# Kernel tuning notes

Measured on AMD Instinct MI355X. Metric: run time of the kernel, lower is better.

Reference implementation:

```python
import jax, jax.numpy as jnp
import numpy as np


def _mab(Q, K, wq, bq, wk, bk, wv, bv, wo, bo, num_heads):
    # Faithful MAB (no LayerNorm: ln=False throughout SetPooler's settrans).
    V = wq.shape[1]
    dh = V // num_heads
    q = Q @ wq + bq          # [..., Sq, V]
    k = K @ wk + bk          # [..., Sk, V]
    v = K @ wv + bv
    def heads(x):
        return x.reshape(*x.shape[:-1], num_heads, dh).swapaxes(-2, -3)  # [..., h, S, dh]
    qh, kh, vh = heads(q), heads(k), heads(v)
    scale = jnp.asarray(1.0 / np.sqrt(V), q.dtype)  # note: torch code scales by sqrt(dim_V), not sqrt(head_dim)
    A = jax.nn.softmax(jnp.einsum('...hqd,...hkd->...hqk', qh, kh) * scale, axis=-1)
    O = qh + jnp.einsum('...hqk,...hkd->...hqd', A, vh)               # residual on Q_
    O = O.swapaxes(-2, -3).reshape(*Q.shape[:-1], V)                  # merge heads back
    return O + jax.nn.relu(O @ wo + bo)


def _forward(rep_R, GA,
             sab0_wq, sab0_bq, sab0_wk, sab0_bk, sab0_wv, sab0_bv, sab0_wo, sab0_bo,
             sab1_wq, sab1_bq, sab1_wk, sab1_bk, sab1_wv, sab1_bv, sab1_wo, sab1_bo,
             pma_S, pma_wq, pma_bq, pma_wk, pma_bk, pma_wv, pma_bv, pma_wo, pma_bo,
             mlp_w1, mlp_b1, mlp_w2, mlp_b2, mlp_w3, mlp_b3):
    # masked mul: GA [G,N] -> [1,G,N,1] broadcast against rep_R [B,G,N,D]
    X = GA[None, :, :, None] * rep_R
    # two SABs (self-attention), 4 heads each
    X = _mab(X, X, sab0_wq, sab0_bq, sab0_wk, sab0_bk, sab0_wv, sab0_bv, sab0_wo, sab0_bo, 4)
    X = _mab(X, X, sab1_wq, sab1_bq, sab1_wk, sab1_bk, sab1_wv, sab1_bv, sab1_wo, sab1_bo, 4)
    # PMA: 1 learned seed, 2 heads, squeeze_out
    S = jnp.broadcast_to(pma_S, (*X.shape[:-2], *pma_S.shape))  # [B,G,1,D]
    O = _mab(S, X, pma_wq, pma_bq, pma_wk, pma_bk, pma_wv, pma_bv, pma_wo, pma_bo, 2)
    O = O[..., 0, :]  # squeeze_out -> [B,G,D]
    # MLP head: D -> 512 -> 512 -> 2*dim_z
    h = jax.nn.relu(O @ mlp_w1 + mlp_b1)
    h = jax.nn.relu(h @ mlp_w2 + mlp_b2)
    return h @ mlp_w3 + mlp_b3


def setup_inputs() -> dict:
    key = jax.random.key(0)
    B, G, N, D = 4, 16, 512, 256
    dz2 = 256  # 2 * dim_z
    ks = iter(jax.random.split(key, 64))
    def lin(fi, fo):
        w = jax.random.normal(next(ks), (fi, fo), jnp.float32) / np.float32(np.sqrt(fi))
        return w, jnp.zeros((fo,), jnp.float32)
    inp = {}
    inp['rep_R'] = jax.random.normal(next(ks), (B, G, N, D), jnp.float32)
    inp['GA'] = jax.random.uniform(next(ks), (G, N), jnp.float32)
    for i in range(2):
        for nm in ('q', 'k', 'v', 'o'):
            w, b = lin(D, D)
            inp[f'sab{i}_w{nm}'] = w
            inp[f'sab{i}_b{nm}'] = b
    inp['pma_S'] = jax.random.normal(next(ks), (1, D), jnp.float32) * np.float32(np.sqrt(6.0 / (1 + D)))
    for nm in ('q', 'k', 'v', 'o'):
        w, b = lin(D, D)
        inp[f'pma_w{nm}'] = w
        inp[f'pma_b{nm}'] = b
    inp['mlp_w1'], inp['mlp_b1'] = lin(D, 512)
    inp['mlp_w2'], inp['mlp_b2'] = lin(512, 512)
    inp['mlp_w3'], inp['mlp_b3'] = lin(512, dz2)
    return inp


def reference(rep_R, GA,
              sab0_wq, sab0_bq, sab0_wk, sab0_bk, sab0_wv, sab0_bv, sab0_wo, sab0_bo,
              sab1_wq, sab1_bq, sab1_wk, sab1_bk, sab1_wv, sab1_bv, sab1_wo, sab1_bo,
              pma_S, pma_wq, pma_bq, pma_wk, pma_bk, pma_wv, pma_bv, pma_wo, pma_bo,
              mlp_w1, mlp_b1, mlp_w2, mlp_b2, mlp_w3, mlp_b3):
    return _forward(rep_R, GA,
                    sab0_wq, sab0_bq, sab0_wk, sab0_bk, sab0_wv, sab0_bv, sab0_wo, sab0_bo,
                    sab1_wq, sab1_bq, sab1_wk, sab1_bk, sab1_wv, sab1_bv, sab1_wo, sab1_bo,
                    pma_S, pma_wq, pma_bq, pma_wk, pma_bk, pma_wv, pma_bv, pma_wo, pma_bo,
                    mlp_w1, mlp_b1, mlp_w2, mlp_b2, mlp_w3, mlp_b3)
```

## Files before the change

kernel.cpp:

```cpp
#include <hip/hip_runtime.h>
#include <hip/hip_bf16.h>

typedef __attribute__((ext_vector_type(4)))  float  f32x4;
typedef __attribute__((ext_vector_type(8)))  __bf16 bf16x8;
typedef __attribute__((ext_vector_type(4)))  __bf16 bf16x4;

#define LOG2E_O16 0.09016844005556021f

__device__ __forceinline__ void gload_lds16(const void* g, void* l) {
  __builtin_amdgcn_global_load_lds(
      (const __attribute__((address_space(1))) void*)g,
      (__attribute__((address_space(3))) void*)l, 16, 0, 0);
}

__global__ __launch_bounds__(256) void scale_kernel(
    const float* __restrict__ rep, const float* __restrict__ GA, __bf16* __restrict__ X)
{
  size_t i = (size_t)blockIdx.x * 256 + threadIdx.x;
  size_t e = i * 4;
  f32x4 r = *(const f32x4*)(rep + e);
  int dn = (int)(e >> 8);
  int n  = dn & 511;
  int g  = (dn >> 9) & 15;
  float ga = GA[g * 512 + n];
  bf16x4 o;
  o[0] = (__bf16)(r[0] * ga); o[1] = (__bf16)(r[1] * ga);
  o[2] = (__bf16)(r[2] * ga); o[3] = (__bf16)(r[3] * ga);
  *(bf16x4*)(X + e) = o;
}

struct WPtrs { const float* w[10]; };
__global__ __launch_bounds__(256) void wconv_kernel(WPtrs ws, __bf16* __restrict__ out)
{
  __shared__ float t[64][65];
  const float* w = ws.w[blockIdx.y];
  __bf16* o = out + (size_t)blockIdx.y * 65536;
  const int tr = (blockIdx.x & 3) * 64, tc = (blockIdx.x >> 2) * 64;
  const int r4 = threadIdx.x >> 6, c = threadIdx.x & 63;
#pragma unroll
  for (int p = 0; p < 16; ++p) {
    int row = p * 4 + r4;
    t[row][c] = w[(size_t)(tr + row) * 256 + tc + c];
  }
  __syncthreads();
#pragma unroll
  for (int p = 0; p < 16; ++p) {
    int row = p * 4 + r4;
    o[(size_t)(tc + row) * 256 + tr + c] = (__bf16)t[c][row];
  }
}

#define STAGE_T(A_, B_, bmv, bnv, Kv, tt, bb) do {                                 \
    _Pragma("unroll")                                                              \
    for (int r = 0; r < 4; ++r) {                                                  \
      int rowl = r * 32 + (tid >> 3);                                              \
      int sl = (tid & 7) ^ (rowl & 7);                                             \
      gload_lds16((const char*)((A_) + (size_t)((bmv) + rowl) * (Kv) + (tt) * 64) + sl * 16, \
                  (char*)sA + (bb) * 16384 + r * 4096 + wv * 1024);                \
      gload_lds16((const char*)((B_) + (size_t)((bnv) + rowl) * (Kv) + (tt) * 64) + sl * 16, \
                  (char*)sB + (bb) * 16384 + r * 4096 + wv * 1024);                \
    } } while (0)

#define GEMM64_PIPE(A_, B_, bmv, bnv, Kv)                                          \
  f32x4 acc[4][4] = {};                                                            \
  const int nt = (Kv) >> 6;                                                        \
  STAGE_T(A_, B_, bmv, bnv, Kv, 0, 0);                                             \
  asm volatile("s_waitcnt vmcnt(0)" ::: "memory");                                 \
  __builtin_amdgcn_s_barrier();                                                    \
  for (int t = 0; t < nt; ++t) {                                                   \
    if (t + 1 < nt) STAGE_T(A_, B_, bmv, bnv, Kv, t + 1, (t + 1) & 1);             \
    const char* bA = (const char*)sA + (t & 1) * 16384;                            \
    const char* bB = (const char*)sB + (t & 1) * 16384;                            \
    bf16x8 af[4][2], bfr[4][2];                                                    \
    _Pragma("unroll")                                                              \
    for (int mi = 0; mi < 4; ++mi) {                                               \
      int row = wr + mi * 16 + l16;                                                \
      _Pragma("unroll")                                                            \
      for (int kk = 0; kk < 2; ++kk) {                                             \
        int sl = (kk * 4 + lg) ^ (row & 7);                                        \
        af[mi][kk] = *(const bf16x8*)(bA + row * 128 + sl * 16);                   \
      }                                                                            \
    }                                                                              \
    _Pragma("unroll")                                                              \
    for (int ni = 0; ni < 4; ++ni) {                                               \
      int row = wc + ni * 16 + l16;                                                \
      _Pragma("unroll")                                                            \
      for (int kk = 0; kk < 2; ++kk) {                                             \
        int sl = (kk * 4 + lg) ^ (row & 7);                                        \
        bfr[ni][kk] = *(const bf16x8*)(bB + row * 128 + sl * 16);                  \
      }                                                                            \
    }                                                                              \
    _Pragma("unroll")                                                              \
    for (int kk = 0; kk < 2; ++kk)                                                 \
      _Pragma("unroll")                                                            \
      for (int mi = 0; mi < 4; ++mi)                                               \
        _Pragma("unroll")                                                          \
        for (int ni = 0; ni < 4; ++ni)                                             \
          acc[mi][ni] = __builtin_amdgcn_mfma_f32_16x16x32_bf16(                   \
              af[mi][kk], bfr[ni][kk], acc[mi][ni], 0, 0, 0);                      \
    asm volatile("s_waitcnt vmcnt(0)" ::: "memory");                               \
    __builtin_amdgcn_s_barrier();                                                  \
  }

struct QKV3 {
  const __bf16* Bt[3];
  const float* bias[3];
  __bf16* out[3];
};

template<int NW>
__global__ __launch_bounds__(256) void gemmqkv_kernel(
    const __bf16* __restrict__ A, QKV3 args, int K)
{
  __shared__ __align__(16) __bf16 smem[32768];
  __bf16* const sA = smem;
  __bf16* const sB = smem + 16384;
  __bf16* const sC = smem;
  const int tid = threadIdx.x, lane = tid & 63, wv = tid >> 6;
  const int l16 = lane & 15, lg = lane >> 4;
  const int wr = (wv >> 1) * 64, wc = (wv & 1) * 64;

  const int nblk = gridDim.x, cpx = nblk >> 3, orig = blockIdx.x;
  const int wg  = (orig & 7) * cpx + (orig >> 3);
  const int r_  = wg / (2 * NW), rem = wg % (2 * NW);
  const int j   = rem >> 1;
  const int bm  = r_ * 128, bn = (rem & 1) * 128;
  const __bf16* __restrict__ Bt = args.Bt[j];

  GEMM64_PIPE(A, Bt, bm, bn, K)

  const float* bias = args.bias[j];
  __bf16* C = args.out[j];
#pragma unroll
  for (int mi = 0; mi < 4; ++mi)
#pragma unroll
    for (int ni = 0; ni < 4; ++ni) {
      int cl = wc + ni * 16 + l16;
      float bval = bias[bn + cl];
      int r0 = wr + mi * 16 + lg * 4;
#pragma unroll
      for (int i = 0; i < 4; ++i)
        sC[(r0 + i) * 136 + cl] = (__bf16)(acc[mi][ni][i] + bval);
    }
  __syncthreads();
#pragma unroll
  for (int it = 0; it < 8; ++it) {
    int idx = it * 256 + tid;
    int r = idx >> 4, seg = idx & 15;
    bf16x8 cv = *(const bf16x8*)&sC[r * 136 + seg * 8];
    *(bf16x8*)(C + (size_t)(bm + r) * 256 + bn + seg * 8) = cv;
  }
}

__global__ __launch_bounds__(256) void gemm128_kernel(
    const __bf16* __restrict__ A, const __bf16* __restrict__ Bt,
    const float* __restrict__ bias, const __bf16* __restrict__ R,
    __bf16* __restrict__ C, int K)
{
  __shared__ __align__(16) __bf16 smem[32768];
  __bf16* const sA = smem;
  __bf16* const sB = smem + 16384;
  __bf16* const sC = smem;
  const int tid = threadIdx.x, lane = tid & 63, wv = tid >> 6;
  const int l16 = lane & 15, lg = lane >> 4;
  const int wr = (wv >> 1) * 64, wc = (wv & 1) * 64;

  const int nblk = gridDim.x, cpx = nblk >> 3, orig = blockIdx.x;
  const int wg  = (orig & 7) * cpx + (orig >> 3);
  const int bm  = (wg >> 1) * 128, bn = (wg & 1) * 128;

  GEMM64_PIPE(A, Bt, bm, bn, K)

  const float* __restrict__ biasp = bias;
#pragma unroll
  for (int mi = 0; mi < 4; ++mi)
#pragma unroll
    for (int ni = 0; ni < 4; ++ni) {
      int cl = wc + ni * 16 + l16;
      float bval = biasp[bn + cl];
      int r0 = wr + mi * 16 + lg * 4;
#pragma unroll
      for (int i = 0; i < 4; ++i)
        sC[(r0 + i) * 136 + cl] = (__bf16)fmaxf(acc[mi][ni][i] + bval, 0.f);
    }
  __syncthreads();
#pragma unroll
  for (int it = 0; it < 8; ++it) {
    int idx = it * 256 + tid;
    int r = idx >> 4, seg = idx & 15;
    bf16x8 cv = *(const bf16x8*)&sC[r * 136 + seg * 8];
    bf16x8 rv = *(const bf16x8*)(R + (size_t)(bm + r) * 256 + bn + seg * 8);
    bf16x8 ov;
#pragma unroll
    for (int i = 0; i < 8; ++i)
      ov[i] = (__bf16)((float)rv[i] + (float)cv[i]);
    *(bf16x8*)(C + (size_t)(bm + r) * 256 + bn + seg * 8) = ov;
  }
}

template<int EPI, bool OUTF32>
__global__ __launch_bounds__(256) void gemm_kernel(
    const __bf16* __restrict__ A, const float* __restrict__ B,
    const float* __restrict__ bias, const __bf16* __restrict__ R,
    void* __restrict__ Cv, int M, int N, int K)
{
  __shared__ __bf16 sA[64][40];
  __shared__ __bf16 sB[64][40];
  const int tid  = threadIdx.x;
  const int lane = tid & 63;
  const int wv   = tid >> 6;
  const int wr   = (wv >> 1) * 32;
  const int wc   = (wv & 1) * 32;
  const int bm   = blockIdx.x * 64;
  const int bn   = blockIdx.y * 64;
  const int l16  = lane & 15;
  const int lk8  = (lane >> 4) * 8;

  const int a_r = tid >> 2, a_c = (tid & 3) * 8;
  const int b_c = tid & 63, b_k = (tid >> 6) * 8;

  f32x4 acc[2][2] = {};

  for (int k0 = 0; k0 < K; k0 += 32) {
    bf16x8 av = *(const bf16x8*)(A + (size_t)(bm + a_r) * K + k0 + a_c);
    float bvf[8];
#pragma unroll
    for (int j = 0; j < 8; ++j)
      bvf[j] = B[(size_t)(k0 + b_k + j) * N + bn + b_c];
    *(bf16x8*)&sA[a_r][a_c] = av;
    bf16x8 bb;
#pragma unroll
    for (int j = 0; j < 8; ++j) bb[j] = (__bf16)bvf[j];
    *(bf16x8*)&sB[b_c][b_k] = bb;
    __syncthreads();
    bf16x8 af0 = *(const bf16x8*)&sA[wr + l16][lk8];
    bf16x8 af1 = *(const bf16x8*)&sA[wr + 16 + l16][lk8];
    bf16x8 bf0 = *(const bf16x8*)&sB[wc + l16][lk8];
    bf16x8 bf1 = *(const bf16x8*)&sB[wc + 16 + l16][lk8];
    acc[0][0] = __builtin_amdgcn_mfma_f32_16x16x32_bf16(af0, bf0, acc[0][0], 0, 0, 0);
    acc[0][1] = __builtin_amdgcn_mfma_f32_16x16x32_bf16(af0, bf1, acc[0][1], 0, 0, 0);
    acc[1][0] = __builtin_amdgcn_mfma_f32_16x16x32_bf16(af1, bf0, acc[1][0], 0, 0, 0);
    acc[1][1] = __builtin_amdgcn_mfma_f32_16x16x32_bf16(af1, bf1, acc[1][1], 0, 0, 0);
    __syncthreads();
  }

#pragma unroll
  for (int mi = 0; mi < 2; ++mi)
#pragma unroll
    for (int ni = 0; ni < 2; ++ni) {
      int col = bn + wc + ni * 16 + l16;
      float bval = bias[col];
      int row0 = bm + wr + mi * 16 + (lane >> 4) * 4;
#pragma unroll
      for (int i = 0; i < 4; ++i) {
        int row = row0 + i;
        float v = acc[mi][ni][i] + bval;
        if (EPI == 1) v = fmaxf(v, 0.f);
        if (EPI == 2) v = (float)R[(size_t)row * N + col] + fmaxf(v, 0.f);
        if (OUTF32) ((float*)Cv)[(size_t)row * N + col] = v;
        else        ((__bf16*)Cv)[(size_t)row * N + col] = (__bf16)v;
      }
    }
}

__global__ __launch_bounds__(512, 2) void attn_sab_kernel(
    __bf16* __restrict__ Q, const __bf16* __restrict__ Kb, const __bf16* __restrict__ Vb)
{
  __shared__ __align__(16) __bf16 sK[128][72];
  __shared__ __align__(16) __bf16 sV[64][136];
  __shared__ __align__(16) __bf16 sP[8][16][72];

  const int orig = blockIdx.x;
  const int wg   = (orig & 7) * 64 + (orig >> 3);
  const int qh   = wg & 1;
  const int pair = wg >> 1;
  const int head = pair & 3;
  const int item = pair >> 2;

  const int tid  = threadIdx.x;
  const int lane = tid & 63;
  const int wv   = tid >> 6;
  const int l16  = lane & 15;
  const int lg   = lane >> 4;
  const size_t base = (size_t)item * (512 * 256) + (size_t)head * 64;
  const int qrow0 = qh * 256 + wv * 32;

  bf16x8 aq[2][2];
#pragma unroll
  for (int qb = 0; qb < 2; ++qb) {
    const size_t qrow = base + (size_t)(qrow0 + qb * 16 + l16) * 256;
    aq[qb][0] = *(const bf16x8*)(Q + qrow + lg * 8);
    aq[qb][1] = *(const bf16x8*)(Q + qrow + 32 + lg * 8);
  }

  f32x4 acco[2][4] = {};
  float lsum[2] = {0.f, 0.f};

  const int kr  = tid >> 3, kc8 = (tid & 7) * 8;
  const int vch = tid & 63, vk8 = (tid >> 6) * 8;

  bf16x8 kreg[2], vreg[2];

#define LOADC(cc) do {                                                             \
    _Pragma("unroll")                                                              \
    for (int p = 0; p < 2; ++p) {                                                  \
      kreg[p] = *(const bf16x8*)(Kb + base + (size_t)((cc)*128 + p*64 + kr)*256 + kc8); \
      bf16x8 vv;                                                                   \
      _Pragma("unroll")                                                            \
      for (int jj = 0; jj < 8; ++jj)                                               \
        vv[jj] = Vb[base + (size_t)((cc)*128 + p*64 + vk8 + jj)*256 + vch];        \
      vreg[p] = vv;                                                                \
    } } while (0)

  LOADC(0);

  for (int c = 0; c < 4; ++c) {
    if (c) __syncthreads();
#pragma unroll
    for (int p = 0; p < 2; ++p) {
      *(bf16x8*)&sK[p * 64 + kr][kc8] = kreg[p];
      *(bf16x8*)&sV[vch][p * 64 + vk8] = vreg[p];
    }
    __syncthreads();
    if (c < 3) LOADC(c + 1);

#pragma unroll
    for (int half = 0; half < 2; ++half) {
      bf16x8 kf0[4], kf1[4];
#pragma unroll
      for (int st = 0; st < 4; ++st) {
        int krl = half * 64 + st * 16 + l16;
        kf0[st] = *(const bf16x8*)&sK[krl][lg * 8];
        kf1[st] = *(const bf16x8*)&sK[krl][32 + lg * 8];
      }
      bf16x8 vf[2][4];
#pragma unroll
      for (int kk = 0; kk < 2; ++kk)
#pragma unroll
        for (int vt = 0; vt < 4; ++vt)
          vf[kk][vt] = *(const bf16x8*)&sV[vt * 16 + l16][half * 64 + kk * 32 + lg * 8];

#pragma unroll
      for (int qb = 0; qb < 2; ++qb) {
        f32x4 s[4];
#pragma unroll
        for (int st = 0; st < 4; ++st) {
          f32x4 z = {};
          s[st] = __builtin_amdgcn_mfma_f32_16x16x32_bf16(kf0[st], aq[qb][0], z, 0, 0, 0);
        }
#pragma unroll
        for (int st = 0; st < 4; ++st)
          s[st] = __builtin_amdgcn_mfma_f32_16x16x32_bf16(kf1[st], aq[qb][1], s[st], 0, 0, 0);
#pragma unroll
        for (int st = 0; st < 4; ++st) {
          bf16x4 pv4;
          float ls = 0.f;
#pragma unroll
          for (int i = 0; i < 4; ++i) {
            float p = __builtin_amdgcn_exp2f(s[st][i] * LOG2E_O16);
            ls += p;
            pv4[i] = (__bf16)p;
          }
          lsum[qb] += ls;
          *(bf16x4*)&sP[wv][l16][st * 16 + lg * 4] = pv4;
        }
#pragma unroll
        for (int kk = 0; kk < 2; ++kk) {
          bf16x8 ap = *(const bf16x8*)&sP[wv][l16][kk * 32 + lg * 8];
#pragma unroll
          for (int vt = 0; vt < 4; ++vt)
            acco[qb][vt] = __builtin_amdgcn_mfma_f32_16x16x32_bf16(ap, vf[kk][vt], acco[qb][vt], 0, 0, 0);
        }
      }
    }
  }
#undef LOADC

#pragma unroll
  for (int qb = 0; qb < 2; ++qb) {
    float t = lsum[qb];
    t += __shfl_xor(t, 16, 64);
    t += __shfl_xor(t, 32, 64);
#pragma unroll
    for (int i = 0; i < 4; ++i) {
      float tot = __shfl(t, lg * 4 + i, 64);
      float inv = 1.0f / tot;
      int row = qrow0 + qb * 16 + lg * 4 + i;
#pragma unroll
      for (int vt = 0; vt < 4; ++vt) {
        size_t idx = base + (size_t)row * 256 + vt * 16 + l16;
        Q[idx] = (__bf16)((float)Q[idx] + acco[qb][vt][i] * inv);
      }
    }
  }
}

__global__ __launch_bounds__(256) void pma_attn_kernel(
    const float* __restrict__ S, const float* __restrict__ wq,
    const float* __restrict__ bq, const __bf16* __restrict__ Kb,
    const __bf16* __restrict__ Vb, __bf16* __restrict__ Opma)
{
  __shared__ float sS[256];
  __shared__ float sq[256];
  __shared__ float sP[512];
  __shared__ float wsum[4];
  __shared__ float sl0;
  __shared__ float red[256];

  const int item = blockIdx.x >> 2;
  const int quarter = blockIdx.x & 3;
  const int h = quarter >> 1;
  const int t = threadIdx.x;
  const int lane = t & 63, wv = t >> 6;

  sS[t] = S[t];
  __syncthreads();
  {
    float acc = bq[t];
#pragma unroll 8
    for (int k = 0; k < 256; ++k) acc += sS[k] * wq[k * 256 + t];
    sq[t] = acc;
  }
  __syncthreads();

#pragma unroll
  for (int rep = 0; rep < 2; ++rep) {
    int key = rep * 256 + t;
    const __bf16* kr = Kb + ((size_t)item * 512 + key) * 256 + h * 128;
    float s = 0.f;
#pragma unroll
    for (int d8 = 0; d8 < 128; d8 += 8) {
      bf16x8 kv = *(const bf16x8*)(kr + d8);
#pragma unroll
      for (int j = 0; j < 8; ++j) s += sq[h * 128 + d8 + j] * (float)kv[j];
    }
    sP[key] = __builtin_amdgcn_exp2f(s * LOG2E_O16);
  }
  __syncthreads();

  {
    float p = sP[t] + sP[t + 256];
#pragma unroll
    for (int m = 1; m < 64; m <<= 1) p += __shfl_xor(p, m, 64);
    if (lane == 0) wsum[wv] = p;
  }
  __syncthreads();
  if (t == 0) sl0 = 1.0f / (wsum[0] + wsum[1] + wsum[2] + wsum[3]);

  {
    const int chl = t & 63, seg = t >> 6;
    const int ch = quarter * 64 + chl;
    const __bf16* vp = Vb + ((size_t)item * 512 + seg * 128) * 256 + ch;
    float acc = 0.f;
#pragma unroll 4
    for (int k = 0; k < 128; ++k)
      acc += sP[seg * 128 + k] * (float)vp[(size_t)k * 256];
    red[t] = acc;
  }
  __syncthreads();
  if (t < 64) {
    int ch = quarter * 64 + t;
    float a = red[t] + red[t + 64] + red[t + 128] + red[t + 192];
    Opma[item * 256 + ch] = (__bf16)(sq[ch] + a * sl0);
  }
}

extern "C" void kernel_launch(void* const* d_in, const int* in_sizes, int n_in,
                              void* d_out, int out_size, void* d_ws, size_t ws_size,
                              hipStream_t stream)
{
  const size_t XSZ = (size_t)64 * 512 * 256;
  if (ws_size < 4 * XSZ * sizeof(__bf16) + (4u << 20)) return;

  const float* rep = (const float*)d_in[0];
  const float* GA  = (const float*)d_in[1];

  __bf16* X    = (__bf16*)d_ws;
  __bf16* Qb   = X  + XSZ;
  __bf16* Kb   = Qb + XSZ;
  __bf16* Vb   = Kb + XSZ;
  __bf16* wT   = Vb + XSZ;
  __bf16* Opma = wT + 10 * 65536;
  __bf16* O2   = Opma + 64 * 256;
  __bf16* H1   = O2 + 64 * 256;
  __bf16* H2   = H1 + 64 * 512;

  WPtrs wp;
  for (int s = 0; s < 2; ++s)
    for (int j = 0; j < 4; ++j)
      wp.w[s * 4 + j] = (const float*)d_in[2 + s * 8 + j * 2];
  wp.w[8] = (const float*)d_in[21];
  wp.w[9] = (const float*)d_in[23];
  wconv_kernel<<<dim3(16, 10), 256, 0, stream>>>(wp, wT);

  scale_kernel<<<8192, 256, 0, stream>>>(rep, GA, X);

  for (int sab = 0; sab < 2; ++sab) {
    QKV3 a;
    a.Bt[0] = wT + (size_t)(sab * 4 + 0) * 65536;
    a.Bt[1] = wT + (size_t)(sab * 4 + 1) * 65536;
    a.Bt[2] = wT + (size_t)(sab * 4 + 2) * 65536;
    a.bias[0] = (const float*)d_in[2 + sab * 8 + 1];
    a.bias[1] = (const float*)d_in[2 + sab * 8 + 3];
    a.bias[2] = (const float*)d_in[2 + sab * 8 + 5];
    a.out[0] = Qb; a.out[1] = Kb; a.out[2] = Vb;
    gemmqkv_kernel<3><<<1536, 256, 0, stream>>>(X, a, 256);
    attn_sab_kernel<<<512, 512, 0, stream>>>(Qb, Kb, Vb);
    gemm128_kernel<<<512, 256, 0, stream>>>(Qb, wT + (size_t)(sab * 4 + 3) * 65536,
        (const float*)d_in[2 + sab * 8 + 7], Qb, X, 256);
  }

  {
    QKV3 a;
    a.Bt[0] = wT + (size_t)8 * 65536;
    a.Bt[1] = wT + (size_t)9 * 65536;
    a.Bt[2] = wT;
    a.bias[0] = (const float*)d_in[22];
    a.bias[1] = (const float*)d_in[24];
    a.bias[2] = (const float*)d_in[22];
    a.out[0] = Kb; a.out[1] = Vb; a.out[2] = Kb;
    gemmqkv_kernel<2><<<1024, 256, 0, stream>>>(X, a, 256);
  }
  pma_attn_kernel<<<256, 256, 0, stream>>>((const float*)d_in[18], (const float*)d_in[19],
      (const float*)d_in[20], Kb, Vb, Opma);
  gemm_kernel<2, false><<<dim3(1, 4), 256, 0, stream>>>(Opma, (const float*)d_in[25],
      (const float*)d_in[26], Opma, O2, 64, 256, 256);
  gemm_kernel<1, false><<<dim3(1, 8), 256, 0, stream>>>(O2, (const float*)d_in[27],
      (const float*)d_in[28], nullptr, H1, 64, 512, 256);
  gemm_kernel<1, false><<<dim3(1, 8), 256, 0, stream>>>(H1, (const float*)d_in[29],
      (const float*)d_in[30], nullptr, H2, 64, 512, 512);
  gemm_kernel<0, true><<<dim3(1, 4), 256, 0, stream>>>(H2, (const float*)d_in[31],
      (const float*)d_in[32], nullptr, (float*)d_out, 64, 256, 512);
}
```

Baseline: 218.7 us.

## Fuse PMA output projection and MLP head into one per-item kernel

Measured after the change: 233.9 us. 1.07x slower.

```diff
diff --git a/kernel.cpp b/kernel.cpp
--- a/kernel.cpp
+++ b/kernel.cpp
@@ -198,71 +198,6 @@
   }
 }
 
-template<int EPI, bool OUTF32>
-__global__ __launch_bounds__(256) void gemm_kernel(
-    const __bf16* __restrict__ A, const float* __restrict__ B,
-    const float* __restrict__ bias, const __bf16* __restrict__ R,
-    void* __restrict__ Cv, int M, int N, int K)
-{
-  __shared__ __bf16 sA[64][40];
-  __shared__ __bf16 sB[64][40];
-  const int tid  = threadIdx.x;
-  const int lane = tid & 63;
-  const int wv   = tid >> 6;
-  const int wr   = (wv >> 1) * 32;
-  const int wc   = (wv & 1) * 32;
-  const int bm   = blockIdx.x * 64;
-  const int bn   = blockIdx.y * 64;
-  const int l16  = lane & 15;
-  const int lk8  = (lane >> 4) * 8;
-
-  const int a_r = tid >> 2, a_c = (tid & 3) * 8;
-  const int b_c = tid & 63, b_k = (tid >> 6) * 8;
-
-  f32x4 acc[2][2] = {};
-
-  for (int k0 = 0; k0 < K; k0 += 32) {
-    bf16x8 av = *(const bf16x8*)(A + (size_t)(bm + a_r) * K + k0 + a_c);
-    float bvf[8];
-#pragma unroll
-    for (int j = 0; j < 8; ++j)
-      bvf[j] = B[(size_t)(k0 + b_k + j) * N + bn + b_c];
-    *(bf16x8*)&sA[a_r][a_c] = av;
-    bf16x8 bb;
-#pragma unroll
-    for (int j = 0; j < 8; ++j) bb[j] = (__bf16)bvf[j];
-    *(bf16x8*)&sB[b_c][b_k] = bb;
-    __syncthreads();
-    bf16x8 af0 = *(const bf16x8*)&sA[wr + l16][lk8];
-    bf16x8 af1 = *(const bf16x8*)&sA[wr + 16 + l16][lk8];
-    bf16x8 bf0 = *(const bf16x8*)&sB[wc + l16][lk8];
-    bf16x8 bf1 = *(const bf16x8*)&sB[wc + 16 + l16][lk8];
-    acc[0][0] = __builtin_amdgcn_mfma_f32_16x16x32_bf16(af0, bf0, acc[0][0], 0, 0, 0);
-    acc[0][1] = __builtin_amdgcn_mfma_f32_16x16x32_bf16(af0, bf1, acc[0][1], 0, 0, 0);
-    acc[1][0] = __builtin_amdgcn_mfma_f32_16x16x32_bf16(af1, bf0, acc[1][0], 0, 0, 0);
-    acc[1][1] = __builtin_amdgcn_mfma_f32_16x16x32_bf16(af1, bf1, acc[1][1], 0, 0, 0);
-    __syncthreads();
-  }
-
-#pragma unroll
-  for (int mi = 0; mi < 2; ++mi)
-#pragma unroll
-    for (int ni = 0; ni < 2; ++ni) {
-      int col = bn + wc + ni * 16 + l16;
-      float bval = bias[col];
-      int row0 = bm + wr + mi * 16 + (lane >> 4) * 4;
-#pragma unroll
-      for (int i = 0; i < 4; ++i) {
-        int row = row0 + i;
-        float v = acc[mi][ni][i] + bval;
-        if (EPI == 1) v = fmaxf(v, 0.f);
-        if (EPI == 2) v = (float)R[(size_t)row * N + col] + fmaxf(v, 0.f);
-        if (OUTF32) ((float*)Cv)[(size_t)row * N + col] = v;
-        else        ((__bf16*)Cv)[(size_t)row * N + col] = (__bf16)v;
-      }
-    }
-}
-
 __global__ __launch_bounds__(512, 2) void attn_sab_kernel(
     __bf16* __restrict__ Q, const __bf16* __restrict__ Kb, const __bf16* __restrict__ Vb)
 {
@@ -465,6 +400,72 @@
   }
 }
 
+__global__ __launch_bounds__(512) void mlp_fused_kernel(
+    const __bf16* __restrict__ Opma,
+    const float* __restrict__ wo, const float* __restrict__ bo,
+    const float* __restrict__ w1, const float* __restrict__ b1,
+    const float* __restrict__ w2, const float* __restrict__ b2,
+    const float* __restrict__ w3, const float* __restrict__ b3,
+    float* __restrict__ out)
+{
+  __shared__ float xO[256];
+  __shared__ float xO2[256];
+  __shared__ float h1[512];
+  __shared__ float h2[512];
+  __shared__ float part[512];
+
+  const int item = blockIdx.x;
+  const int t = threadIdx.x;
+
+  if (t < 256) xO[t] = (float)Opma[item * 256 + t];
+  __syncthreads();
+
+  {
+    const int j = t & 255, kh = t >> 8;
+    float s = 0.f;
+#pragma unroll 8
+    for (int k = kh * 128; k < kh * 128 + 128; ++k)
+      s += xO[k] * wo[(size_t)k * 256 + j];
+    part[t] = s;
+  }
+  __syncthreads();
+  if (t < 256) {
+    float v = part[t] + part[t + 256] + bo[t];
+    xO2[t] = xO[t] + fmaxf(v, 0.f);
+  }
+  __syncthreads();
+
+  {
+    float s = b1[t];
+#pragma unroll 8
+    for (int k = 0; k < 256; ++k)
+      s += xO2[k] * w1[(size_t)k * 512 + t];
+    h1[t] = fmaxf(s, 0.f);
+  }
+  __syncthreads();
+
+  {
+    float s = b2[t];
+#pragma unroll 8
+    for (int k = 0; k < 512; ++k)
+      s += h1[k] * w2[(size_t)k * 512 + t];
+    h2[t] = fmaxf(s, 0.f);
+  }
+  __syncthreads();
+
+  {
+    const int j = t & 255, kh = t >> 8;
+    float s = 0.f;
+#pragma unroll 8
+    for (int k = kh * 256; k < kh * 256 + 256; ++k)
+      s += h2[k] * w3[(size_t)k * 256 + j];
+    part[t] = s;
+  }
+  __syncthreads();
+  if (t < 256)
+    out[item * 256 + t] = part[t] + part[t + 256] + b3[t];
+}
+
 extern "C" void kernel_launch(void* const* d_in, const int* in_sizes, int n_in,
                               void* d_out, int out_size, void* d_ws, size_t ws_size,
                               hipStream_t stream)
@@ -481,9 +482,6 @@
   __bf16* Vb   = Kb + XSZ;
   __bf16* wT   = Vb + XSZ;
   __bf16* Opma = wT + 10 * 65536;
-  __bf16* O2   = Opma + 64 * 256;
-  __bf16* H1   = O2 + 64 * 256;
-  __bf16* H2   = H1 + 64 * 512;
 
   WPtrs wp;
   for (int s = 0; s < 2; ++s)
@@ -523,12 +521,10 @@
   }
   pma_attn_kernel<<<256, 256, 0, stream>>>((const float*)d_in[18], (const float*)d_in[19],
       (const float*)d_in[20], Kb, Vb, Opma);
-  gemm_kernel<2, false><<<dim3(1, 4), 256, 0, stream>>>(Opma, (const float*)d_in[25],
-      (const float*)d_in[26], Opma, O2, 64, 256, 256);
-  gemm_kernel<1, false><<<dim3(1, 8), 256, 0, stream>>>(O2, (const float*)d_in[27],
-      (const float*)d_in[28], nullptr, H1, 64, 512, 256);
-  gemm_kernel<1, false><<<dim3(1, 8), 256, 0, stream>>>(H1, (const float*)d_in[29],
-      (const float*)d_in[30], nullptr, H2, 64, 512, 512);
-  gemm_kernel<0, true><<<dim3(1, 4), 256, 0, stream>>>(H2, (const float*)d_in[31],
-      (const float*)d_in[32], nullptr, (float*)d_out, 64, 256, 512);
-}
+  mlp_fused_kernel<<<64, 512, 0, stream>>>(Opma,
+      (const float*)d_in[25], (const float*)d_in[26],
+      (const float*)d_in[27], (const float*)d_in[28],
+      (const float*)d_in[29], (const float*)d_in[30],
+      (const float*)d_in[31], (const float*)d_in[32],
+      (float*)d_out);
+}
```
